# Optimization experiments

Measured on AMD Instinct MI355X. Metric: run time of the kernel, lower is better.

The kernel has to match this reference:

```python
import jax, jax.numpy as jnp
import numpy as np

D_MODEL = 1024
N_HEADS = 16
HEAD_DIM = D_MODEL // N_HEADS  # 64


def setup_inputs() -> dict:
    key = jax.random.key(0)
    k1, k2, k3 = jax.random.split(key, 3)
    x = jax.random.normal(k1, (2, 2048, D_MODEL), dtype=jnp.float32)
    # nn.Linear(d, 3d, bias=False): store transposed so y = x @ W
    w_qkv = jax.random.normal(k2, (D_MODEL, 3 * D_MODEL), dtype=jnp.float32) * (D_MODEL ** -0.5)
    w_proj = jax.random.normal(k3, (D_MODEL, D_MODEL), dtype=jnp.float32) * (D_MODEL ** -0.5)
    return {"x": x, "w_qkv": w_qkv, "w_proj": w_proj}


def reference(x, w_qkv, w_proj):
    b, n, _ = x.shape
    qkv = x @ w_qkv  # [b, n, 3*d_model]
    # einops 'b n (h d qkv) -> qkv b h n d': qkv axis is innermost of the split
    qkv = qkv.reshape(b, n, N_HEADS, HEAD_DIM, 3)
    q = jnp.moveaxis(qkv[..., 0], 1, 2)  # [b, h, n, d]
    k = jnp.moveaxis(qkv[..., 1], 1, 2)
    v = jnp.moveaxis(qkv[..., 2], 1, 2)
    scale = HEAD_DIM ** -0.5
    scores = jnp.einsum('bhqd,bhkd->bhqk', q, k) * scale  # [b, h, n, n]
    causal = jnp.tril(jnp.ones((n, n), dtype=bool))
    scores = jnp.where(causal[None, None], scores, -jnp.inf)
    attn = jax.nn.softmax(scores, axis=-1)
    out = jnp.einsum('bhqk,bhkd->bhqd', attn, v)  # [b, h, n, d]
    out = jnp.moveaxis(out, 1, 2).reshape(b, n, D_MODEL)  # 'b h n d -> b n (h d)'
    return out @ w_proj
```

## Files before the change

kernel.cpp:

```cpp
#include <hip/hip_runtime.h>
#include <cstdint>
#include <cstddef>

#define D_MODEL 1024
#define N_HEADS 16
#define HEAD_DIM 64
#define SEQ 2048
#define BATCH 2

typedef __attribute__((ext_vector_type(8))) short bf16x8;
typedef __attribute__((ext_vector_type(4))) float f32x4;

__device__ inline unsigned short f2bf(float f) {
    union { float f; unsigned u; } v; v.f = f;
    unsigned r = v.u + 0x7fffu + ((v.u >> 16) & 1u);
    return (unsigned short)(r >> 16);
}

__device__ __forceinline__ void gload_lds16(const unsigned short* g, unsigned short* l) {
    __builtin_amdgcn_global_load_lds(
        (const __attribute__((address_space(1))) unsigned int*)g,
        (__attribute__((address_space(3))) unsigned int*)l, 16, 0, 0);
}

__global__ __launch_bounds__(256) void convert_x_kernel(
    const float* __restrict__ X, unsigned short* __restrict__ Xb)
{
    const int idx = blockIdx.x * 256 + threadIdx.x;
    const float4* src = (const float4*)X;
    float4 v0 = src[idx * 2], v1 = src[idx * 2 + 1];
    union { unsigned short u[8]; uint4 v; } o;
    o.u[0] = f2bf(v0.x); o.u[1] = f2bf(v0.y); o.u[2] = f2bf(v0.z); o.u[3] = f2bf(v0.w);
    o.u[4] = f2bf(v1.x); o.u[5] = f2bf(v1.y); o.u[6] = f2bf(v1.z); o.u[7] = f2bf(v1.w);
    ((uint4*)Xb)[idx] = o.v;
}

__global__ __launch_bounds__(256) void convert_transpose_qkv(
    const float* __restrict__ W, unsigned short* __restrict__ Wt)
{
    __shared__ float t[32][33];
    const int c0 = blockIdx.x * 32, r0 = blockIdx.y * 32;
    const int a = threadIdx.x & 31, b = threadIdx.x >> 5;
#pragma unroll
    for (int i = 0; i < 32; i += 8)
        t[b + i][a] = W[(size_t)(r0 + b + i) * (3 * D_MODEL) + c0 + a];
    __syncthreads();
#pragma unroll
    for (int i = 0; i < 32; i += 8) {
        const int c = c0 + b + i;
        const int np = (c % 3) * 1024 + c / 3;
        Wt[(size_t)np * D_MODEL + r0 + a] = f2bf(t[a][b + i]);
    }
}

__global__ __launch_bounds__(256) void convert_transpose_kernel(
    const float* __restrict__ W, unsigned short* __restrict__ Wt,
    int ncols, int nrows)
{
    __shared__ float t[32][33];
    const int c0 = blockIdx.x * 32, r0 = blockIdx.y * 32;
    const int a = threadIdx.x & 31, b = threadIdx.x >> 5;
#pragma unroll
    for (int i = 0; i < 32; i += 8)
        t[b + i][a] = W[(size_t)(r0 + b + i) * ncols + c0 + a];
    __syncthreads();
#pragma unroll
    for (int i = 0; i < 32; i += 8)
        Wt[(size_t)(c0 + b + i) * nrows + r0 + a] = f2bf(t[a][b + i]);
}

__global__ __launch_bounds__(256) void v_transpose(
    const unsigned short* __restrict__ V, unsigned short* __restrict__ Vt)
{
    const int n0 = blockIdx.x * 64;
    const int bh = blockIdx.y;
    __shared__ unsigned short t[64 * 72];
    const int tid = threadIdx.x;
    const uint4* src = (const uint4*)(V + ((size_t)bh * SEQ + n0) * HEAD_DIM);
#pragma unroll
    for (int it = 0; it < 2; it++) {
        const int lin = tid + it * 256;
        const int row = lin >> 3, p = lin & 7;
        ((uint4*)t)[row * 9 + p] = src[lin];
    }
    __syncthreads();
#pragma unroll
    for (int it = 0; it < 2; it++) {
        const int lin = tid + it * 256;
        const int drow = lin >> 3, p = lin & 7;
        union { unsigned short u[8]; uint4 v; } o;
#pragma unroll
        for (int e = 0; e < 8; e++) o.u[e] = t[(p * 8 + e) * 72 + drow];
        ((uint4*)(Vt + ((size_t)bh * HEAD_DIM + drow) * SEQ + n0))[p] = o.v;
    }
}

#define GEMM_MFMA_BODY(A_, B_, Kdim)                                           \
    const int tid = threadIdx.x;                                               \
    const int w = tid >> 6, lane = tid & 63;                                   \
    const int l15 = lane & 15, quad = lane >> 4;                               \
    const int wr = w >> 1, wc = w & 1;                                         \
    const int row0 = blockIdx.y * 128, col0 = blockIdx.x * 128;                \
    __shared__ unsigned short As[2][8192];                                     \
    __shared__ unsigned short Bs[2][8192];                                     \
    const f32x4 zero4 = {0.f, 0.f, 0.f, 0.f};                                  \
    f32x4 acc[4][4];                                                           \
    _Pragma("unroll") for (int i = 0; i < 4; i++)                              \
        _Pragma("unroll") for (int j = 0; j < 4; j++) acc[i][j] = zero4;       \
    auto stage_ = [&](int sb, int k0) {                                        \
        _Pragma("unroll") for (int i = 0; i < 4; i++) {                        \
            const int fa = w * 4 + i;                                          \
            const int mt = fa >> 1, kh = fa & 1;                               \
            const int kc = k0 + kh * 32 + quad * 8;                            \
            gload_lds16((A_) + (size_t)(row0 + mt * 16 + l15) * (Kdim) + kc,   \
                        &As[sb][fa * 512 + lane * 8]);                         \
            gload_lds16((B_) + (size_t)(col0 + mt * 16 + l15) * (Kdim) + kc,   \
                        &Bs[sb][fa * 512 + lane * 8]);                         \
        }                                                                      \
    };                                                                         \
    stage_(0, 0);                                                              \
    const int KITER = (Kdim) / 64;                                             \
    for (int kt = 0; kt < KITER; kt++) {                                       \
        const int sb = kt & 1;                                                 \
        __syncthreads();                                                       \
        if (kt + 1 < KITER) stage_(sb ^ 1, (kt + 1) * 64);                     \
        _Pragma("unroll") for (int kh = 0; kh < 2; kh++) {                     \
            bf16x8 af[4], bfr[4];                                              \
            _Pragma("unroll") for (int i = 0; i < 4; i++)                      \
                af[i] = *(const bf16x8*)&As[sb][((wr * 4 + i) * 2 + kh) * 512 + lane * 8]; \
            _Pragma("unroll") for (int j = 0; j < 4; j++)                      \
                bfr[j] = *(const bf16x8*)&Bs[sb][((wc * 4 + j) * 2 + kh) * 512 + lane * 8]; \
            _Pragma("unroll") for (int i = 0; i < 4; i++)                      \
                _Pragma("unroll") for (int j = 0; j < 4; j++)                  \
                    acc[i][j] = __builtin_amdgcn_mfma_f32_16x16x32_bf16(       \
                        af[i], bfr[j], acc[i][j], 0, 0, 0);                    \
        }                                                                      \
    }

__global__ __launch_bounds__(256) void gemm_qkv_mfma(
    const unsigned short* __restrict__ A, const unsigned short* __restrict__ B,
    unsigned short* __restrict__ Q, unsigned short* __restrict__ Kq,
    unsigned short* __restrict__ Vb)
{
    GEMM_MFMA_BODY(A, B, D_MODEL)
    const int nbase = col0 + wc * 64;
    const int which = nbase >> 10;
    unsigned short* const dst = (which == 0) ? Q : (which == 1) ? Kq : Vb;
#pragma unroll
    for (int i = 0; i < 4; i++) {
#pragma unroll
        for (int r = 0; r < 4; r++) {
            const int row = row0 + wr * 64 + i * 16 + quad * 4 + r;
            const int bb = row >> 11, n = row & (SEQ - 1);
#pragma unroll
            for (int j = 0; j < 4; j++) {
                const int idx = (nbase + j * 16 + l15) & 1023;
                const int h = idx >> 6, dd = idx & 63;
                dst[(((size_t)(bb * N_HEADS + h)) * SEQ + n) * HEAD_DIM + dd] =
                    f2bf(acc[i][j][r]);
            }
        }
    }
}

__global__ __launch_bounds__(256) void gemm_proj_mfma(
    const unsigned short* __restrict__ A, const unsigned short* __restrict__ B,
    float* __restrict__ C)
{
    GEMM_MFMA_BODY(A, B, D_MODEL)
#pragma unroll
    for (int i = 0; i < 4; i++) {
#pragma unroll
        for (int r = 0; r < 4; r++) {
            const int row = row0 + wr * 64 + i * 16 + quad * 4 + r;
#pragma unroll
            for (int j = 0; j < 4; j++) {
                const int c = col0 + wc * 64 + j * 16 + l15;
                C[(size_t)row * D_MODEL + c] = acc[i][j][r];
            }
        }
    }
}

#define PSTR 72

__global__ __launch_bounds__(256) void flash_attn_kernel(
    const unsigned short* __restrict__ Q,
    const unsigned short* __restrict__ K,
    const unsigned short* __restrict__ Vt,
    unsigned short* __restrict__ O)
{
    const int idx = blockIdx.x;
    const int bh = idx & 31;
    const int qt2 = idx >> 5;
    const int hi = qt2 >> 3, lo = qt2 & 7;
    const int qt = (hi == 0) ? lo : (hi == 1) ? 31 - lo : (hi == 2) ? lo + 8 : 23 - lo;

    const int tid = threadIdx.x;
    const int w = tid >> 6, lane = tid & 63;
    const int l15 = lane & 15, quad = lane >> 4;

    __shared__ unsigned short Ks[2][4096];
    __shared__ unsigned short Vs[2][4096];
    __shared__ unsigned short Ps[4][16 * PSTR];

    bf16x8 qf[2];
    {
        const unsigned short* qrow =
            Q + ((size_t)bh * SEQ + qt * 64 + w * 16 + l15) * HEAD_DIM;
        qf[0] = *(const bf16x8*)(qrow + quad * 8);
        qf[1] = *(const bf16x8*)(qrow + 32 + quad * 8);
    }

    const f32x4 zero4 = {0.f, 0.f, 0.f, 0.f};
    f32x4 o_acc[4] = {zero4, zero4, zero4, zero4};
    float m_i = -1e30f, l_i = 0.f;

    auto stage = [&](int bf, int kt_t) {
        const int key0 = kt_t * 64;
#pragma unroll
        for (int i = 0; i < 2; i++) {
            const int f = w * 2 + i;
            const int ct = f >> 1, kh = f & 1;
            gload_lds16(K + ((size_t)bh * SEQ + key0 + ct * 16 + l15) * HEAD_DIM
                          + kh * 32 + quad * 8,
                        &Ks[bf][f * 512 + lane * 8]);
            gload_lds16(Vt + ((size_t)bh * HEAD_DIM + ct * 16 + l15) * SEQ
                           + key0 + kh * 32 + quad * 8,
                        &Vs[bf][f * 512 + lane * 8]);
        }
    };

    stage(0, 0);
    int buf = 0;

    const int qg = qt * 64 + w * 16 + l15;

    for (int kt = 0; kt <= qt; kt++) {
        __syncthreads();
        if (kt < qt) stage(buf ^ 1, kt + 1);

        f32x4 st[4] = {zero4, zero4, zero4, zero4};
#pragma unroll
        for (int kh = 0; kh < 2; kh++) {
#pragma unroll
            for (int ct = 0; ct < 4; ct++) {
                bf16x8 kf = *(const bf16x8*)&Ks[buf][(ct * 2 + kh) * 512 + lane * 8];
                st[ct] = __builtin_amdgcn_mfma_f32_16x16x32_bf16(kf, qf[kh], st[ct], 0, 0, 0);
            }
        }

        const bool diag = (kt == qt);
        float mt = -1e30f;
#pragma unroll
        for (int ct = 0; ct < 4; ct++) {
#pragma unroll
            for (int r = 0; r < 4; r++) {
                float v = st[ct][r] * 0.125f;
                const int kg = kt * 64 + ct * 16 + quad * 4 + r;
                if (diag && kg > qg) v = -1e30f;
                st[ct][r] = v;
                mt = fmaxf(mt, v);
            }
        }
        mt = fmaxf(mt, __shfl_xor(mt, 16));
        mt = fmaxf(mt, __shfl_xor(mt, 32));

        const float mn = fmaxf(m_i, mt);
        const float alpha = __expf(m_i - mn);
        m_i = mn;

        float ls = 0.f;
#pragma unroll
        for (int ct = 0; ct < 4; ct++) {
            union { unsigned short u[4]; uint2 v; } pk;
#pragma unroll
            for (int r = 0; r < 4; r++) {
                float p = __expf(st[ct][r] - mn);
                ls += p;
                pk.u[r] = f2bf(p);
            }
            *(uint2*)&Ps[w][l15 * PSTR + ct * 16 + quad * 4] = pk.v;
        }
        ls += __shfl_xor(ls, 16);
        ls += __shfl_xor(ls, 32);
        l_i = l_i * alpha + ls;

        float ar[4];
#pragma unroll
        for (int r = 0; r < 4; r++)
            ar[r] = __shfl(alpha, (lane & 48) | (quad * 4 + r));
#pragma unroll
        for (int dt = 0; dt < 4; dt++)
#pragma unroll
            for (int r = 0; r < 4; r++)
                o_acc[dt][r] *= ar[r];

#pragma unroll
        for (int kh = 0; kh < 2; kh++) {
            bf16x8 pa = *(const bf16x8*)&Ps[w][l15 * PSTR + kh * 32 + quad * 8];
#pragma unroll
            for (int dt = 0; dt < 4; dt++) {
                bf16x8 vf = *(const bf16x8*)&Vs[buf][(dt * 2 + kh) * 512 + lane * 8];
                o_acc[dt] = __builtin_amdgcn_mfma_f32_16x16x32_bf16(pa, vf, o_acc[dt], 0, 0, 0);
            }
        }
        buf ^= 1;
    }

    const float linv = 1.0f / l_i;
    float lr[4];
#pragma unroll
    for (int r = 0; r < 4; r++)
        lr[r] = __shfl(linv, (lane & 48) | (quad * 4 + r));

    const int b = bh >> 4, h = bh & 15;
#pragma unroll
    for (int r = 0; r < 4; r++) {
        const int q = qt * 64 + w * 16 + quad * 4 + r;
        unsigned short* orow = O + ((size_t)b * SEQ + q) * D_MODEL + h * HEAD_DIM;
#pragma unroll
        for (int dt = 0; dt < 4; dt++)
            orow[dt * 16 + l15] = f2bf(o_acc[dt][r] * lr[r]);
    }
}

extern "C" void kernel_launch(void* const* d_in, const int* in_sizes, int n_in,
                              void* d_out, int out_size, void* d_ws, size_t ws_size,
                              hipStream_t stream) {
    const float* x      = (const float*)d_in[0];
    const float* w_qkv  = (const float*)d_in[1];
    const float* w_proj = (const float*)d_in[2];
    float* out = (float*)d_out;

    unsigned short* Xb  = (unsigned short*)d_ws;
    unsigned short* Wqt = Xb  + (size_t)4 * 1024 * 1024;
    unsigned short* Wpt = Wqt + (size_t)3 * 1024 * 1024;
    unsigned short* Qb  = Wpt + (size_t)1 * 1024 * 1024;
    unsigned short* Kb  = Qb  + (size_t)4 * 1024 * 1024;
    unsigned short* Vb  = Kb  + (size_t)4 * 1024 * 1024;
    unsigned short* Vtb = Vb  + (size_t)4 * 1024 * 1024;
    unsigned short* Ob  = Vtb + (size_t)4 * 1024 * 1024;

    convert_x_kernel<<<dim3(2048), 256, 0, stream>>>(x, Xb);
    convert_transpose_qkv<<<dim3(3072 / 32, 1024 / 32), 256, 0, stream>>>(w_qkv, Wqt);
    convert_transpose_kernel<<<dim3(1024 / 32, 1024 / 32), 256, 0, stream>>>(
        w_proj, Wpt, D_MODEL, D_MODEL);

    gemm_qkv_mfma<<<dim3(3 * D_MODEL / 128, BATCH * SEQ / 128), 256, 0, stream>>>(
        Xb, Wqt, Qb, Kb, Vb);

    v_transpose<<<dim3(SEQ / 64, BATCH * N_HEADS), 256, 0, stream>>>(Vb, Vtb);

    flash_attn_kernel<<<dim3(SEQ / 64 * BATCH * N_HEADS), 256, 0, stream>>>(
        Qb, Kb, Vtb, Ob);

    gemm_proj_mfma<<<dim3(D_MODEL / 128, BATCH * SEQ / 128), 256, 0, stream>>>(
        Ob, Wpt, out);
}
```

Measured before the change: 229.4 us.

## Fuse conversion kernels, triple-buffer GEMM pipeline, split-K projection GEMM

Merges the three input conversion/transpose kernels into one launch. Rewrites the GEMM main loop to a 3-stage LDS pipeline with K-step 32, using explicit vmcnt waits and raw barriers so loads for two steps ahead overlap compute. Splits the projection GEMM over K into two halves, which doubles its grid from 256 blocks. The partial sums go into the reused Q buffer and a separate add kernel reduces them into the output, which costs extra fp32 traffic and one more launch.

```diff
diff --git a/kernel.cpp b/kernel.cpp
--- a/kernel.cpp
+++ b/kernel.cpp
@@ -23,50 +23,52 @@
         (__attribute__((address_space(3))) unsigned int*)l, 16, 0, 0);
 }
 
-__global__ __launch_bounds__(256) void convert_x_kernel(
-    const float* __restrict__ X, unsigned short* __restrict__ Xb)
-{
-    const int idx = blockIdx.x * 256 + threadIdx.x;
-    const float4* src = (const float4*)X;
-    float4 v0 = src[idx * 2], v1 = src[idx * 2 + 1];
-    union { unsigned short u[8]; uint4 v; } o;
-    o.u[0] = f2bf(v0.x); o.u[1] = f2bf(v0.y); o.u[2] = f2bf(v0.z); o.u[3] = f2bf(v0.w);
-    o.u[4] = f2bf(v1.x); o.u[5] = f2bf(v1.y); o.u[6] = f2bf(v1.z); o.u[7] = f2bf(v1.w);
-    ((uint4*)Xb)[idx] = o.v;
-}
-
-__global__ __launch_bounds__(256) void convert_transpose_qkv(
-    const float* __restrict__ W, unsigned short* __restrict__ Wt)
-{
+#define WAITCNT_VM4 0x0F74
+#define WAITCNT_VM0 0x0F70
+
+__global__ __launch_bounds__(256) void fused_convert_kernel(
+    const float* __restrict__ X, unsigned short* __restrict__ Xb,
+    const float* __restrict__ Wq, unsigned short* __restrict__ Wqt,
+    const float* __restrict__ Wp, unsigned short* __restrict__ Wpt)
+{
+    const int blk = blockIdx.x;
+    const int tid = threadIdx.x;
     __shared__ float t[32][33];
-    const int c0 = blockIdx.x * 32, r0 = blockIdx.y * 32;
-    const int a = threadIdx.x & 31, b = threadIdx.x >> 5;
-#pragma unroll
-    for (int i = 0; i < 32; i += 8)
-        t[b + i][a] = W[(size_t)(r0 + b + i) * (3 * D_MODEL) + c0 + a];
-    __syncthreads();
-#pragma unroll
-    for (int i = 0; i < 32; i += 8) {
-        const int c = c0 + b + i;
-        const int np = (c % 3) * 1024 + c / 3;
-        Wt[(size_t)np * D_MODEL + r0 + a] = f2bf(t[a][b + i]);
-    }
-}
-
-__global__ __launch_bounds__(256) void convert_transpose_kernel(
-    const float* __restrict__ W, unsigned short* __restrict__ Wt,
-    int ncols, int nrows)
-{
-    __shared__ float t[32][33];
-    const int c0 = blockIdx.x * 32, r0 = blockIdx.y * 32;
-    const int a = threadIdx.x & 31, b = threadIdx.x >> 5;
-#pragma unroll
-    for (int i = 0; i < 32; i += 8)
-        t[b + i][a] = W[(size_t)(r0 + b + i) * ncols + c0 + a];
-    __syncthreads();
-#pragma unroll
-    for (int i = 0; i < 32; i += 8)
-        Wt[(size_t)(c0 + b + i) * nrows + r0 + a] = f2bf(t[a][b + i]);
+
+    if (blk < 2048) {
+        const int idx = blk * 256 + tid;
+        const float4* src = (const float4*)X;
+        float4 v0 = src[idx * 2], v1 = src[idx * 2 + 1];
+        union { unsigned short u[8]; uint4 v; } o;
+        o.u[0] = f2bf(v0.x); o.u[1] = f2bf(v0.y); o.u[2] = f2bf(v0.z); o.u[3] = f2bf(v0.w);
+        o.u[4] = f2bf(v1.x); o.u[5] = f2bf(v1.y); o.u[6] = f2bf(v1.z); o.u[7] = f2bf(v1.w);
+        ((uint4*)Xb)[idx] = o.v;
+    } else if (blk < 5120) {
+        const int bb = blk - 2048;
+        const int c0 = (bb % 96) * 32, r0 = (bb / 96) * 32;
+        const int a = tid & 31, b = tid >> 5;
+#pragma unroll
+        for (int i = 0; i < 32; i += 8)
+            t[b + i][a] = Wq[(size_t)(r0 + b + i) * (3 * D_MODEL) + c0 + a];
+        __syncthreads();
+#pragma unroll
+        for (int i = 0; i < 32; i += 8) {
+            const int c = c0 + b + i;
+            const int np = (c % 3) * 1024 + c / 3;
+            Wqt[(size_t)np * D_MODEL + r0 + a] = f2bf(t[a][b + i]);
+        }
+    } else {
+        const int bb = blk - 5120;
+        const int c0 = (bb % 32) * 32, r0 = (bb / 32) * 32;
+        const int a = tid & 31, b = tid >> 5;
+#pragma unroll
+        for (int i = 0; i < 32; i += 8)
+            t[b + i][a] = Wp[(size_t)(r0 + b + i) * D_MODEL + c0 + a];
+        __syncthreads();
+#pragma unroll
+        for (int i = 0; i < 32; i += 8)
+            Wpt[(size_t)(c0 + b + i) * D_MODEL + r0 + a] = f2bf(t[a][b + i]);
+    }
 }
 
 __global__ __launch_bounds__(256) void v_transpose(
@@ -95,46 +97,50 @@
     }
 }
 
-#define GEMM_MFMA_BODY(A_, B_, Kdim)                                           \
+#define GEMM_PIPE3_BODY(A_, B_, KBASE, NITER)                                  \
     const int tid = threadIdx.x;                                               \
     const int w = tid >> 6, lane = tid & 63;                                   \
     const int l15 = lane & 15, quad = lane >> 4;                               \
     const int wr = w >> 1, wc = w & 1;                                         \
     const int row0 = blockIdx.y * 128, col0 = blockIdx.x * 128;                \
-    __shared__ unsigned short As[2][8192];                                     \
-    __shared__ unsigned short Bs[2][8192];                                     \
+    __shared__ unsigned short As[3][4096];                                     \
+    __shared__ unsigned short Bs[3][4096];                                     \
     const f32x4 zero4 = {0.f, 0.f, 0.f, 0.f};                                  \
     f32x4 acc[4][4];                                                           \
     _Pragma("unroll") for (int i = 0; i < 4; i++)                              \
         _Pragma("unroll") for (int j = 0; j < 4; j++) acc[i][j] = zero4;       \
-    auto stage_ = [&](int sb, int k0) {                                        \
-        _Pragma("unroll") for (int i = 0; i < 4; i++) {                        \
-            const int fa = w * 4 + i;                                          \
-            const int mt = fa >> 1, kh = fa & 1;                               \
-            const int kc = k0 + kh * 32 + quad * 8;                            \
-            gload_lds16((A_) + (size_t)(row0 + mt * 16 + l15) * (Kdim) + kc,   \
-                        &As[sb][fa * 512 + lane * 8]);                         \
-            gload_lds16((B_) + (size_t)(col0 + mt * 16 + l15) * (Kdim) + kc,   \
-                        &Bs[sb][fa * 512 + lane * 8]);                         \
+    auto stage_ = [&](int sb, int kt_) {                                       \
+        const int k0 = (KBASE) + kt_ * 32 + quad * 8;                          \
+        _Pragma("unroll") for (int i = 0; i < 2; i++) {                        \
+            const int f = w * 2 + i;                                           \
+            gload_lds16((A_) + (size_t)(row0 + f * 16 + l15) * D_MODEL + k0,   \
+                        &As[sb][f * 512 + lane * 8]);                          \
+            gload_lds16((B_) + (size_t)(col0 + f * 16 + l15) * D_MODEL + k0,   \
+                        &Bs[sb][f * 512 + lane * 8]);                          \
         }                                                                      \
     };                                                                         \
     stage_(0, 0);                                                              \
-    const int KITER = (Kdim) / 64;                                             \
-    for (int kt = 0; kt < KITER; kt++) {                                       \
-        const int sb = kt & 1;                                                 \
-        __syncthreads();                                                       \
-        if (kt + 1 < KITER) stage_(sb ^ 1, (kt + 1) * 64);                     \
-        _Pragma("unroll") for (int kh = 0; kh < 2; kh++) {                     \
-            bf16x8 af[4], bfr[4];                                              \
-            _Pragma("unroll") for (int i = 0; i < 4; i++)                      \
-                af[i] = *(const bf16x8*)&As[sb][((wr * 4 + i) * 2 + kh) * 512 + lane * 8]; \
+    stage_(1, 1);                                                              \
+    int sb = 0;                                                                \
+    for (int kt = 0; kt < (NITER); kt++) {                                     \
+        if (kt < (NITER) - 1) {                                                \
+            __builtin_amdgcn_s_waitcnt(WAITCNT_VM4);                           \
+            __builtin_amdgcn_s_barrier();                                      \
+            if (kt + 2 < (NITER)) stage_((sb + 2 > 2) ? sb - 1 : sb + 2, kt + 2); \
+        } else {                                                               \
+            __builtin_amdgcn_s_waitcnt(WAITCNT_VM0);                           \
+            __builtin_amdgcn_s_barrier();                                      \
+        }                                                                      \
+        bf16x8 af[4], bfr[4];                                                  \
+        _Pragma("unroll") for (int i = 0; i < 4; i++)                          \
+            af[i] = *(const bf16x8*)&As[sb][(wr * 4 + i) * 512 + lane * 8];    \
+        _Pragma("unroll") for (int j = 0; j < 4; j++)                          \
+            bfr[j] = *(const bf16x8*)&Bs[sb][(wc * 4 + j) * 512 + lane * 8];   \
+        _Pragma("unroll") for (int i = 0; i < 4; i++)                          \
             _Pragma("unroll") for (int j = 0; j < 4; j++)                      \
-                bfr[j] = *(const bf16x8*)&Bs[sb][((wc * 4 + j) * 2 + kh) * 512 + lane * 8]; \
-            _Pragma("unroll") for (int i = 0; i < 4; i++)                      \
-                _Pragma("unroll") for (int j = 0; j < 4; j++)                  \
-                    acc[i][j] = __builtin_amdgcn_mfma_f32_16x16x32_bf16(       \
-                        af[i], bfr[j], acc[i][j], 0, 0, 0);                    \
-        }                                                                      \
+                acc[i][j] = __builtin_amdgcn_mfma_f32_16x16x32_bf16(           \
+                    af[i], bfr[j], acc[i][j], 0, 0, 0);                        \
+        sb = (sb == 2) ? 0 : sb + 1;                                           \
     }
 
 __global__ __launch_bounds__(256) void gemm_qkv_mfma(
@@ -142,7 +148,7 @@
     unsigned short* __restrict__ Q, unsigned short* __restrict__ Kq,
     unsigned short* __restrict__ Vb)
 {
-    GEMM_MFMA_BODY(A, B, D_MODEL)
+    GEMM_PIPE3_BODY(A, B, 0, 32)
     const int nbase = col0 + wc * 64;
     const int which = nbase >> 10;
     unsigned short* const dst = (which == 0) ? Q : (which == 1) ? Kq : Vb;
@@ -163,11 +169,13 @@
     }
 }
 
-__global__ __launch_bounds__(256) void gemm_proj_mfma(
+__global__ __launch_bounds__(256) void gemm_proj_splitk(
     const unsigned short* __restrict__ A, const unsigned short* __restrict__ B,
-    float* __restrict__ C)
-{
-    GEMM_MFMA_BODY(A, B, D_MODEL)
+    float* __restrict__ P)
+{
+    const int kbase = blockIdx.z * 512;
+    GEMM_PIPE3_BODY(A, B, kbase, 16)
+    float* const dst = P + (size_t)blockIdx.z * (4096ull * 1024ull);
 #pragma unroll
     for (int i = 0; i < 4; i++) {
 #pragma unroll
@@ -176,9 +184,24 @@
 #pragma unroll
             for (int j = 0; j < 4; j++) {
                 const int c = col0 + wc * 64 + j * 16 + l15;
-                C[(size_t)row * D_MODEL + c] = acc[i][j][r];
-            }
-        }
+                dst[(size_t)row * D_MODEL + c] = acc[i][j][r];
+            }
+        }
+    }
+}
+
+__global__ __launch_bounds__(256) void add_out_kernel(
+    const float* __restrict__ P, float* __restrict__ out)
+{
+    const float4* p0 = (const float4*)P;
+    const float4* p1 = (const float4*)(P + 4096ull * 1024ull);
+    float4* o = (float4*)out;
+    const int base = (blockIdx.x * 256 + threadIdx.x) * 4;
+#pragma unroll
+    for (int j = 0; j < 4; j++) {
+        float4 a = p0[base + j], b = p1[base + j];
+        float4 r = {a.x + b.x, a.y + b.y, a.z + b.z, a.w + b.w};
+        o[base + j] = r;
     }
 }
 
@@ -342,10 +365,10 @@
     unsigned short* Vtb = Vb  + (size_t)4 * 1024 * 1024;
     unsigned short* Ob  = Vtb + (size_t)4 * 1024 * 1024;
 
-    convert_x_kernel<<<dim3(2048), 256, 0, stream>>>(x, Xb);
-    convert_transpose_qkv<<<dim3(3072 / 32, 1024 / 32), 256, 0, stream>>>(w_qkv, Wqt);
-    convert_transpose_kernel<<<dim3(1024 / 32, 1024 / 32), 256, 0, stream>>>(
-        w_proj, Wpt, D_MODEL, D_MODEL);
+    float* Pp = (float*)Qb;
+
+    fused_convert_kernel<<<dim3(6144), 256, 0, stream>>>(
+        x, Xb, w_qkv, Wqt, w_proj, Wpt);
 
     gemm_qkv_mfma<<<dim3(3 * D_MODEL / 128, BATCH * SEQ / 128), 256, 0, stream>>>(
         Xb, Wqt, Qb, Kb, Vb);
@@ -355,6 +378,8 @@
     flash_attn_kernel<<<dim3(SEQ / 64 * BATCH * N_HEADS), 256, 0, stream>>>(
         Qb, Kb, Vtb, Ob);
 
-    gemm_proj_mfma<<<dim3(D_MODEL / 128, BATCH * SEQ / 128), 256, 0, stream>>>(
-        Ob, Wpt, out);
-}
+    gemm_proj_splitk<<<dim3(D_MODEL / 128, BATCH * SEQ / 128, 2), 256, 0, stream>>>(
+        Ob, Wpt, Pp);
+
+    add_out_kernel<<<dim3(1024), 256, 0, stream>>>(Pp, out);
+}
```

New measurement: 221.4 us. 3.5% less time.
